# Kernel tuning notes

Hardware: AMD Instinct MI355X
Metric: run time of the kernel (lower is better)

## Reference

```python
import jax, jax.numpy as jnp
import numpy as np

B, T, D, H, L, W = 32, 512, 256, 8, 2, 10
NQ = 10000
HD = D // H


def setup_inputs():
    key = jax.random.key(0)
    ks = jax.random.split(key, 16)
    def n(k, shape, s=0.02):
        return jax.random.normal(k, shape, jnp.float32) * s
    return {
        "q": jax.random.randint(ks[0], (B, T), 0, NQ),
        "s": jax.random.randint(ks[1], (B, T), 0, 2),
        "q_embed": n(ks[2], (NQ + 1, D)),
        "s_embed": n(ks[3], (2, D)),
        "pos_embed": n(ks[4], (512, D)),
        "fusion_w": n(ks[5], (2 * D, D)),
        "fusion_b": jnp.zeros((D,), jnp.float32),
        "in_proj_w": n(ks[6], (L, D, 3 * D)),
        "in_proj_b": jnp.zeros((L, 3 * D), jnp.float32),
        "out_proj_w": n(ks[7], (L, D, D)),
        "out_proj_b": jnp.zeros((L, D), jnp.float32),
        "ln1_g": jnp.ones((L, D), jnp.float32),
        "ln1_b": jnp.zeros((L, D), jnp.float32),
        "ln2_g": jnp.ones((L, D), jnp.float32),
        "ln2_b": jnp.zeros((L, D), jnp.float32),
        "ff1_w": n(ks[8], (L, D, 4 * D)),
        "ff1_b": jnp.zeros((L, 4 * D), jnp.float32),
        "ff2_w": n(ks[9], (L, 4 * D, D)),
        "ff2_b": jnp.zeros((L, D), jnp.float32),
        "sw1": n(ks[10], (6, 32), 0.1),
        "sb1": jnp.zeros((32,), jnp.float32),
        "sw2": n(ks[11], (32, D // 4), 0.1),
        "sb2": jnp.zeros((D // 4,), jnp.float32),
        "cw1": n(ks[12], (D + D // 4, D)),
        "cb1": jnp.zeros((D,), jnp.float32),
        "cw2": n(ks[13], (D, 1)),
        "cb2": jnp.zeros((1,), jnp.float32),
    }


def _ln(x, g, b):
    mu = jnp.mean(x, -1, keepdims=True)
    var = jnp.mean(jnp.square(x - mu), -1, keepdims=True)
    return (x - mu) * jax.lax.rsqrt(var + 1e-5) * g + b


def _sliding_sum(x, w):
    # sum over trailing window of size w ending at each t, via prefix sums
    c = jnp.concatenate([jnp.zeros((x.shape[0], 1), x.dtype), jnp.cumsum(x, axis=1)], axis=1)
    t = jnp.arange(x.shape[1])
    return c[:, t + 1] - c[:, jnp.maximum(t + 1 - w, 0)]


def _stats(s, mask):
    # vectorized version of _extract_statistics (prefix-sum sliding windows)
    mf = mask.astype(jnp.float32)
    sf = s.astype(jnp.float32) * mf
    valid = _sliding_sum(mf, W)
    correct_rate = _sliding_sum(sf, W) / (valid + 1e-6)
    rc = _sliding_sum(mf, 5)
    recent_correct = _sliding_sum(sf, 5) / (rc + 1e-6)
    trans = ((s[:, 1:] != s[:, :-1]) & mask[:, 1:] & mask[:, :-1]).astype(jnp.float32)
    diff = jnp.concatenate([jnp.zeros((s.shape[0], 1), jnp.float32), trans], axis=1)
    change_rate = _sliding_sum(diff, W - 1) / (valid + 1e-6)
    # max consecutive equal run within each trailing window of size W
    sp = jnp.pad(s, ((0, 0), (W - 1, 0)))
    mp = jnp.pad(mask, ((0, 0), (W - 1, 0)))
    win_s = [sp[:, j:j + T] for j in range(W)]
    win_m = [mp[:, j:j + T] for j in range(W)]
    run = win_m[0].astype(jnp.float32)
    mx = run
    for j in range(1, W):  # fixed small window, not a data-dim loop
        eq = (win_s[j] == win_s[j - 1]) & win_m[j - 1]
        run = win_m[j].astype(jnp.float32) * (jnp.where(eq, run, 0.0) + 1.0)
        mx = jnp.maximum(mx, run)
    rel = jnp.broadcast_to(jnp.arange(T, dtype=jnp.float32) / max(T, 100), s.shape)
    cov = valid / W
    return jnp.stack([correct_rate, recent_correct, change_rate, mx / W, rel, cov], axis=-1)


def reference(q, s, q_embed, s_embed, pos_embed, fusion_w, fusion_b, in_proj_w, in_proj_b,
              out_proj_w, out_proj_b, ln1_g, ln1_b, ln2_g, ln2_b, ff1_w, ff1_b, ff2_w, ff2_b,
              sw1, sb1, sw2, sb2, cw1, cb1, cw2, cb2):
    mask = s >= 0
    qm = jnp.where(mask, q, 0)
    sm = jnp.where(mask, s, 0)
    h = jnp.concatenate([q_embed[qm], s_embed[sm]], axis=-1)  # [B,T,2D]
    h = jax.nn.relu(h @ fusion_w + fusion_b) + pos_embed[:T][None]
    causal = jnp.tril(jnp.ones((T, T), bool))
    allowed = causal[None, None] & mask[:, None, None, :]
    scale = 1.0 / (HD ** 0.5)
    for l in range(L):
        qkv = h @ in_proj_w[l] + in_proj_b[l]
        qh, kh, vh = jnp.split(qkv, 3, axis=-1)
        qh = qh.reshape(B, T, H, HD).transpose(0, 2, 1, 3)
        kh = kh.reshape(B, T, H, HD).transpose(0, 2, 1, 3)
        vh = vh.reshape(B, T, H, HD).transpose(0, 2, 1, 3)
        scores = jnp.einsum('bhqd,bhkd->bhqk', qh, kh) * scale
        scores = jnp.where(allowed, scores, -1e9)
        attn = jax.nn.softmax(scores, axis=-1)
        o = jnp.einsum('bhqk,bhkd->bhqd', attn, vh).transpose(0, 2, 1, 3).reshape(B, T, D)
        h = _ln(h + (o @ out_proj_w[l] + out_proj_b[l]), ln1_g[l], ln1_b[l])
        ff = jax.nn.gelu(h @ ff1_w[l] + ff1_b[l], approximate=False) @ ff2_w[l] + ff2_b[l]
        h = _ln(h + ff, ln2_g[l], ln2_b[l])
    sfeat = _stats(sm, mask)  # [B,T,6]
    semb = jax.nn.relu(sfeat @ sw1 + sb1) @ sw2 + sb2  # [B,T,D//4]
    comb = jnp.concatenate([h, semb], axis=-1)
    logits = (jax.nn.relu(comb @ cw1 + cb1) @ cw2 + cb2)[..., 0]
    return jnp.where(mask, logits, -1e9)
```

## Files before the change

### kernel.cpp

```cpp
#include <hip/hip_runtime.h>
#include <hip/hip_bf16.h>
#include <cmath>


using short8 = __attribute__((ext_vector_type(8))) short;
using short4v = __attribute__((ext_vector_type(4))) short;
using f32x4  = __attribute__((ext_vector_type(4))) float;

__device__ inline float gelu_f(float x) {
    return 0.5f * x * (1.0f + erff(x * 0.70710678118654752f));
}

__device__ inline short f2bf(float x) {
    union { float f; unsigned u; } v; v.f = x;
    return (short)((v.u + 0x7fffu + ((v.u >> 16) & 1u)) >> 16);
}

__device__ inline unsigned packbf(float lo, float hi) {
    union { float f; unsigned u; } a, b; a.f = lo; b.f = hi;
    unsigned ra = (a.u + 0x7fffu + ((a.u >> 16) & 1u)) >> 16;
    unsigned rb = (b.u + 0x7fffu + ((b.u >> 16) & 1u)) >> 16;
    return (rb << 16) | (ra & 0xffffu);
}

__device__ inline float wave_reduce_sum(float v) {
#pragma unroll
    for (int off = 32; off > 0; off >>= 1) v += __shfl_xor(v, off);
    return v;
}

#define GLOAD16(gp, lp) __builtin_amdgcn_global_load_lds( \
    (const __attribute__((address_space(1))) void*)(gp), \
    (__attribute__((address_space(3))) void*)(lp), 16, 0, 0)

__global__ __launch_bounds__(256) void transpose_all(
    const float* __restrict__ fusion_w, const float* __restrict__ in_proj_w,
    const float* __restrict__ out_proj_w, const float* __restrict__ ff1_w,
    const float* __restrict__ ff2_w, const float* __restrict__ cw1,
    short* __restrict__ wts)
{
    const int b0[10]      = {0,128,320,512,576,640,896,1152,1408,1664};
    const int Ks[10]      = {512,256,256,256,256,256,256,1024,1024,320};
    const int Ns[10]      = {256,768,768,256,256,1024,1024,256,256,256};
    const int sidx[10]    = {0,1,1,2,2,3,3,4,4,5};
    const size_t soff[10] = {0,0,196608,0,65536,0,262144,0,262144,0};
    const size_t doff[10] = {0,131072,327680,524288,589824,655360,917504,1179648,1441792,1703936};
    const float* srcs[6] = {fusion_w, in_proj_w, out_proj_w, ff1_w, ff2_w, cw1};

    int bid = blockIdx.x;
    int mi = 0;
    while (mi < 9 && bid >= b0[mi + 1]) ++mi;
    int bl = bid - b0[mi];
    int K = Ks[mi], N = Ns[mi];
    int tx = bl % (N >> 5), ty = bl / (N >> 5);
    const float* src = srcs[sidx[mi]] + soff[mi];
    short* dst = wts + doff[mi];

    __shared__ float tile[32][33];
    int c = threadIdx.x & 31, r = threadIdx.x >> 5;
#pragma unroll
    for (int i = 0; i < 4; ++i)
        tile[r + i * 8][c] = src[(size_t)(ty * 32 + r + i * 8) * N + tx * 32 + c];
    __syncthreads();
#pragma unroll
    for (int i = 0; i < 4; ++i)
        dst[(size_t)(tx * 32 + r + i * 8) * K + ty * 32 + c] = f2bf(tile[c][r + i * 8]);
}

__global__ __launch_bounds__(256) void embed_gather_bf16(
    const int* __restrict__ q, const int* __restrict__ s,
    const float* __restrict__ qe, const float* __restrict__ se,
    short* __restrict__ A)
{
    int e8 = blockIdx.x * 256 + threadIdx.x;
    int row = e8 >> 6;
    int k8 = (e8 & 63) << 3;
    int sv = s[row];
    bool mk = sv >= 0;
    const float* src = (k8 < 256) ? qe + (size_t)(mk ? q[row] : 0) * 256 + k8
                                  : se + (size_t)(mk ? sv : 0) * 256 + (k8 - 256);
    float4 v0 = *(const float4*)src;
    float4 v1 = *(const float4*)(src + 4);
    short8 o;
    o[0] = f2bf(v0.x); o[1] = f2bf(v0.y); o[2] = f2bf(v0.z); o[3] = f2bf(v0.w);
    o[4] = f2bf(v1.x); o[5] = f2bf(v1.y); o[6] = f2bf(v1.z); o[7] = f2bf(v1.w);
    *(short8*)(A + (size_t)row * 512 + k8) = o;
}

template<int EPI>
__global__ __launch_bounds__(512) void gemm512(
    const short* __restrict__ A, const short* __restrict__ A2,
    const short* __restrict__ Wt, const float* __restrict__ bias,
    float* __restrict__ hf, short* __restrict__ hb,
    short* __restrict__ oq, short* __restrict__ ok, short* __restrict__ ov,
    const float* __restrict__ gamma, const float* __restrict__ beta,
    const float* __restrict__ pos,
    const float* __restrict__ cw2, const float* __restrict__ cb2,
    const int* __restrict__ smask, float* __restrict__ outlog,
    int N, int K)
{
    const int tid = threadIdx.x, lane = tid & 63, wv = tid >> 6;
    const int lg = lane >> 4, lr = lane & 15;
    const int wr = wv >> 2, wc = wv & 3;
    const int m0 = blockIdx.y * 64, n0 = blockIdx.x * 256;

    __shared__ short As[2][2048];
    __shared__ short Bs[2][8192];
    __shared__ float redS[64][4];
    __shared__ float redQ[64][4];

    f32x4 acc[2][4] = {};
    const int nsteps = K >> 5;

    auto stage = [&](int buf, int step) {
        int k0 = step << 5;
        if (tid < 256) {
            int k = k0 + wv * 8;
            const short* srcA;
            if (EPI == 4) srcA = (k < 256) ? A  + (size_t)(m0 + lane) * 256 + k
                                           : A2 + (size_t)(m0 + lane) * 64 + (k - 256);
            else          srcA = A + (size_t)(m0 + lane) * K + k;
            GLOAD16(srcA, &As[buf][(wv * 64) * 8]);
        }
        {
            int g = tid >> 8, n = tid & 255;
            GLOAD16(Wt + (size_t)(n0 + n) * K + k0 + g * 8, &Bs[buf][(wv * 64) * 8]);
        }
        {
            int slot = tid + 512;
            int g = slot >> 8, n = slot & 255;
            GLOAD16(Wt + (size_t)(n0 + n) * K + k0 + g * 8, &Bs[buf][((wv + 8) * 64) * 8]);
        }
    };

    stage(0, 0);
    __syncthreads();
    for (int step = 0; step < nsteps; ++step) {
        int cur = step & 1;
        if (step + 1 < nsteps) stage(cur ^ 1, step + 1);
        short8 a[2], b[4];
#pragma unroll
        for (int i = 0; i < 2; ++i)
            a[i] = *(const short8*)&As[cur][(lg * 64 + wr * 32 + i * 16 + lr) * 8];
#pragma unroll
        for (int j = 0; j < 4; ++j)
            b[j] = *(const short8*)&Bs[cur][(lg * 256 + wc * 64 + j * 16 + lr) * 8];
#pragma unroll
        for (int i = 0; i < 2; ++i)
#pragma unroll
            for (int j = 0; j < 4; ++j)
                acc[i][j] = __builtin_amdgcn_mfma_f32_16x16x32_bf16(a[i], b[j], acc[i][j], 0, 0, 0);
        __syncthreads();
    }

    if (EPI == 0) {
#pragma unroll
        for (int i = 0; i < 2; ++i)
#pragma unroll
        for (int j = 0; j < 4; ++j)
#pragma unroll
        for (int r = 0; r < 4; ++r) {
            int row = m0 + wr * 32 + i * 16 + lg * 4 + r;
            int col = wc * 64 + j * 16 + lr;
            float x = acc[i][j][r] + bias[col];
            x = fmaxf(x, 0.f) + pos[(size_t)(row & 511) * 256 + col];
            hf[(size_t)row * 256 + col] = x;
            hb[(size_t)row * 256 + col] = f2bf(x);
        }
    } else if (EPI == 1) {
        const int sec = blockIdx.x;
#pragma unroll
        for (int i = 0; i < 2; ++i)
#pragma unroll
        for (int j = 0; j < 4; ++j)
#pragma unroll
        for (int r = 0; r < 4; ++r) {
            int row = m0 + wr * 32 + i * 16 + lg * 4 + r;
            int col = wc * 64 + j * 16 + lr;
            int t = row & 511, bg = row >> 9;
            int h = col >> 5, d = col & 31, bh = bg * 8 + h;
            short v = f2bf(acc[i][j][r] + bias[n0 + col]);
            if (sec == 0)      oq[((size_t)bh * 512 + t) * 32 + d] = v;
            else if (sec == 1) ok[((size_t)bh * 512 + t) * 32 + d] = v;
            else {
                int kl = t & 31;
                ov[(size_t)bh * 16384 + (size_t)(t >> 5) * 1024 +
                   (size_t)((kl >> 2) & 3) * 256 + d * 8 + (((kl & 3) << 1) | ((kl >> 4) & 1))] = v;
            }
        }
    } else if (EPI == 2) {
#pragma unroll
        for (int i = 0; i < 2; ++i)
#pragma unroll
        for (int j = 0; j < 4; ++j)
#pragma unroll
        for (int r = 0; r < 4; ++r) {
            int row = m0 + wr * 32 + i * 16 + lg * 4 + r;
            int col = n0 + wc * 64 + j * 16 + lr;
            float x = acc[i][j][r] + bias[col];
            oq[(size_t)row * N + col] = f2bf(gelu_f(x));
        }
    } else if (EPI == 3) {
        float ps[2][4], pq[2][4];
#pragma unroll
        for (int i = 0; i < 2; ++i)
#pragma unroll
        for (int r = 0; r < 4; ++r) { ps[i][r] = 0.f; pq[i][r] = 0.f; }
#pragma unroll
        for (int i = 0; i < 2; ++i)
#pragma unroll
        for (int j = 0; j < 4; ++j)
#pragma unroll
        for (int r = 0; r < 4; ++r) {
            int row = m0 + wr * 32 + i * 16 + lg * 4 + r;
            int col = wc * 64 + j * 16 + lr;
            float x = acc[i][j][r] + bias[col] + hf[(size_t)row * 256 + col];
            acc[i][j][r] = x;
            ps[i][r] += x; pq[i][r] += x * x;
        }
#pragma unroll
        for (int off = 1; off < 16; off <<= 1)
#pragma unroll
            for (int i = 0; i < 2; ++i)
#pragma unroll
            for (int r = 0; r < 4; ++r) {
                ps[i][r] += __shfl_xor(ps[i][r], off);
                pq[i][r] += __shfl_xor(pq[i][r], off);
            }
        if (lr == 0) {
#pragma unroll
            for (int i = 0; i < 2; ++i)
#pragma unroll
            for (int r = 0; r < 4; ++r) {
                int rl = wr * 32 + i * 16 + lg * 4 + r;
                redS[rl][wc] = ps[i][r]; redQ[rl][wc] = pq[i][r];
            }
        }
        __syncthreads();
#pragma unroll
        for (int i = 0; i < 2; ++i)
#pragma unroll
        for (int r = 0; r < 4; ++r) {
            int rl = wr * 32 + i * 16 + lg * 4 + r;
            int row = m0 + rl;
            float sm = redS[rl][0] + redS[rl][1] + redS[rl][2] + redS[rl][3];
            float sq = redQ[rl][0] + redQ[rl][1] + redQ[rl][2] + redQ[rl][3];
            float mu = sm * (1.f / 256.f);
            float var = sq * (1.f / 256.f) - mu * mu;
            float rstd = rsqrtf(var + 1e-5f);
#pragma unroll
            for (int j = 0; j < 4; ++j) {
                int col = wc * 64 + j * 16 + lr;
                float y = (acc[i][j][r] - mu) * rstd * gamma[col] + beta[col];
                hf[(size_t)row * 256 + col] = y;
                hb[(size_t)row * 256 + col] = f2bf(y);
            }
        }
    } else {
        float p[2][4];
#pragma unroll
        for (int i = 0; i < 2; ++i)
#pragma unroll
        for (int r = 0; r < 4; ++r) p[i][r] = 0.f;
#pragma unroll
        for (int i = 0; i < 2; ++i)
#pragma unroll
        for (int j = 0; j < 4; ++j)
#pragma unroll
        for (int r = 0; r < 4; ++r) {
            int col = wc * 64 + j * 16 + lr;
            float x = fmaxf(acc[i][j][r] + bias[col], 0.f);
            p[i][r] += x * cw2[col];
        }
#pragma unroll
        for (int off = 1; off < 16; off <<= 1)
#pragma unroll
            for (int i = 0; i < 2; ++i)
#pragma unroll
            for (int r = 0; r < 4; ++r) p[i][r] += __shfl_xor(p[i][r], off);
        if (lr == 0) {
#pragma unroll
            for (int i = 0; i < 2; ++i)
#pragma unroll
            for (int r = 0; r < 4; ++r)
                redS[wr * 32 + i * 16 + lg * 4 + r][wc] = p[i][r];
        }
        __syncthreads();
        if (tid < 64) {
            int row = m0 + tid;
            float v = redS[tid][0] + redS[tid][1] + redS[tid][2] + redS[tid][3] + cb2[0];
            outlog[row] = (smask[row] >= 0) ? v : -1e9f;
        }
    }
}

__global__ __launch_bounds__(256) void attn_mfma(
    const short* __restrict__ Qg, const short* __restrict__ Kg,
    const short* __restrict__ VTg, short* __restrict__ O)
{
    __shared__ unsigned Wp[4][16][20];
    const int bh = blockIdx.x >> 2, part = blockIdx.x & 3;
    const int b = bh >> 3, h = bh & 7;
    const int wv = threadIdx.x >> 6, lane = threadIdx.x & 63;
    const int lg = lane >> 4, lr = lane & 15;
    const int slot = part * 4 + wv;
    const short* Qbh = Qg + (size_t)bh * 16384;
    const short* Kbh = Kg + (size_t)bh * 16384;
    const short* Vbh = VTg + (size_t)bh * 16384;
    const float scale = 0.17677669529663687f;

    for (int half = 0; half < 2; ++half) {
        const int tile = half ? (31 - slot) : slot;
        const int q0 = tile << 4;
        short8 qa = *(const short8*)(Qbh + (size_t)(q0 + lr) * 32 + lg * 8);
        f32x4 o0 = {}, o1 = {};
        float l_[4] = {0.f, 0.f, 0.f, 0.f};
        const int nfull = q0 >> 5;

        for (int c = 0; c <= nfull; ++c) {
            int kc = c << 5;
            short8 kf0 = *(const short8*)(Kbh + (size_t)(kc + lr) * 32 + lg * 8);
            short8 kf1 = *(const short8*)(Kbh + (size_t)(kc + 16 + lr) * 32 + lg * 8);
            f32x4 s0 = {}, s1 = {};
            s0 = __builtin_amdgcn_mfma_f32_16x16x32_bf16(qa, kf0, s0, 0, 0, 0);
            s1 = __builtin_amdgcn_mfma_f32_16x16x32_bf16(qa, kf1, s1, 0, 0, 0);
            float p0[4], p1[4];
            if (c < nfull) {
#pragma unroll
                for (int r = 0; r < 4; ++r) {
                    p0[r] = __expf(s0[r] * scale);
                    p1[r] = __expf(s1[r] * scale);
                }
            } else {
#pragma unroll
                for (int r = 0; r < 4; ++r) {
                    int qq = q0 + lg * 4 + r;
                    p0[r] = (kc + lr)      > qq ? 0.f : __expf(s0[r] * scale);
                    p1[r] = (kc + 16 + lr) > qq ? 0.f : __expf(s1[r] * scale);
                }
            }
#pragma unroll
            for (int r = 0; r < 4; ++r) {
                l_[r] += p0[r] + p1[r];
                Wp[wv][lg * 4 + r][lr] = packbf(p0[r], p1[r]);
            }
            short8 pa = *(const short8*)&Wp[wv][lr][lg * 4];
            short8 vf0 = *(const short8*)(Vbh + (size_t)c * 1024 + lg * 256 + lr * 8);
            short8 vf1 = *(const short8*)(Vbh + (size_t)c * 1024 + lg * 256 + (lr + 16) * 8);
            o0 = __builtin_amdgcn_mfma_f32_16x16x32_bf16(pa, vf0, o0, 0, 0, 0);
            o1 = __builtin_amdgcn_mfma_f32_16x16x32_bf16(pa, vf1, o1, 0, 0, 0);
        }
#pragma unroll
        for (int off = 1; off < 16; off <<= 1)
#pragma unroll
            for (int r = 0; r < 4; ++r) l_[r] += __shfl_xor(l_[r], off);
#pragma unroll
        for (int r = 0; r < 4; ++r) {
            float inv = 1.f / l_[r];
            size_t ro = ((size_t)b * 512 + q0 + lg * 4 + r) * 256 + h * 32;
            O[ro + lr] = f2bf(o0[r] * inv);
            O[ro + 16 + lr] = f2bf(o1[r] * inv);
        }
    }
}

__global__ __launch_bounds__(512) void stats_kernel(
    const int* __restrict__ s, short* __restrict__ semb,
    const float* __restrict__ sw1, const float* __restrict__ sb1,
    const float* __restrict__ sw2, const float* __restrict__ sb2)
{
    __shared__ float sv_sh[512];
    __shared__ float m_sh[512];
    __shared__ float sw2_sh[2048];
    const int b = blockIdx.x;
    const int t = threadIdx.x;
    {
        int sval = s[b * 512 + t];
        bool mk = sval >= 0;
        sv_sh[t] = mk ? (float)sval : 0.f;
        m_sh[t] = mk ? 1.f : 0.f;
    }
    for (int i = t; i < 2048; i += 512) sw2_sh[i] = sw2[i];
    __syncthreads();

    float mf10 = 0, sf10 = 0, mf5 = 0, sf5 = 0, d9 = 0;
#pragma unroll
    for (int k = 0; k < 10; ++k) {
        int idx = t - k;
        if (idx >= 0) {
            float mv = m_sh[idx], sv = sv_sh[idx];
            mf10 += mv; sf10 += sv;
            if (k < 5) { mf5 += mv; sf5 += sv; }
            if (k < 9 && idx >= 1) {
                if (sv != sv_sh[idx - 1] && mv > 0.5f && m_sh[idx - 1] > 0.5f) d9 += 1.f;
            }
        }
    }
    float run, mx;
    {
        int x0 = t - 9;
        run = (x0 >= 0) ? m_sh[x0] : 0.f;
        mx = run;
#pragma unroll
        for (int j = 1; j < 10; ++j) {
            int xc = t + j - 9, xp = xc - 1;
            float sc = (xc >= 0) ? sv_sh[xc] : 0.f;
            float sp = (xp >= 0) ? sv_sh[xp] : 0.f;
            float mc = (xc >= 0) ? m_sh[xc] : 0.f;
            float mp = (xp >= 0) ? m_sh[xp] : 0.f;
            bool eq = (sc == sp) && (mp > 0.5f);
            run = (mc > 0.5f) ? ((eq ? run : 0.f) + 1.f) : 0.f;
            mx = fmaxf(mx, run);
        }
    }
    float f[6];
    f[0] = sf10 / (mf10 + 1e-6f);
    f[1] = sf5 / (mf5 + 1e-6f);
    f[2] = d9 / (mf10 + 1e-6f);
    f[3] = mx * 0.1f;
    f[4] = (float)t * (1.f / 512.f);
    f[5] = mf10 * 0.1f;

    float hid[32];
#pragma unroll
    for (int j2 = 0; j2 < 32; ++j2) {
        float a = sb1[j2];
#pragma unroll
        for (int i = 0; i < 6; ++i) a = fmaf(f[i], sw1[i * 32 + j2], a);
        hid[j2] = fmaxf(a, 0.f);
    }
    short* orow = semb + ((size_t)b * 512 + t) * 64;
    for (int c = 0; c < 64; c += 4) {
        float v0 = sb2[c], v1 = sb2[c + 1], v2 = sb2[c + 2], v3 = sb2[c + 3];
#pragma unroll
        for (int j2 = 0; j2 < 32; ++j2) {
            float hh = hid[j2];
            v0 = fmaf(hh, sw2_sh[j2 * 64 + c], v0);
            v1 = fmaf(hh, sw2_sh[j2 * 64 + c + 1], v1);
            v2 = fmaf(hh, sw2_sh[j2 * 64 + c + 2], v2);
            v3 = fmaf(hh, sw2_sh[j2 * 64 + c + 3], v3);
        }
        short4v o; o[0] = f2bf(v0); o[1] = f2bf(v1); o[2] = f2bf(v2); o[3] = f2bf(v3);
        *(short4v*)(orow + c) = o;
    }
}

extern "C" void kernel_launch(void* const* d_in, const int* in_sizes, int n_in,
                              void* d_out, int out_size, void* d_ws, size_t ws_size,
                              hipStream_t stream) {
    const int*   q         = (const int*)d_in[0];
    const int*   s         = (const int*)d_in[1];
    const float* q_embed   = (const float*)d_in[2];
    const float* s_embed   = (const float*)d_in[3];
    const float* pos_embed = (const float*)d_in[4];
    const float* fusion_w  = (const float*)d_in[5];
    const float* fusion_b  = (const float*)d_in[6];
    const float* in_proj_w = (const float*)d_in[7];
    const float* in_proj_b = (const float*)d_in[8];
    const float* out_proj_w= (const float*)d_in[9];
    const float* out_proj_b= (const float*)d_in[10];
    const float* ln1_g     = (const float*)d_in[11];
    const float* ln1_b     = (const float*)d_in[12];
    const float* ln2_g     = (const float*)d_in[13];
    const float* ln2_b     = (const float*)d_in[14];
    const float* ff1_w     = (const float*)d_in[15];
    const float* ff1_b     = (const float*)d_in[16];
    const float* ff2_w     = (const float*)d_in[17];
    const float* ff2_b     = (const float*)d_in[18];
    const float* sw1       = (const float*)d_in[19];
    const float* sb1       = (const float*)d_in[20];
    const float* sw2       = (const float*)d_in[21];
    const float* sb2       = (const float*)d_in[22];
    const float* cw1       = (const float*)d_in[23];
    const float* cb1       = (const float*)d_in[24];
    const float* cw2       = (const float*)d_in[25];
    const float* cb2       = (const float*)d_in[26];
    float* out = (float*)d_out;

    char* base = (char*)d_ws;
    float* hf   = (float*)(base);
    short* hb   = (short*)(base + 16777216);
    short* bufA = (short*)(base + 25165824);
    short* att  = (short*)(base + 58720256);
    short* Qg   = (short*)(base + 67108864);
    short* Kg   = (short*)(base + 75497472);
    short* VTg  = (short*)(base + 83886080);
    short* semb = (short*)(base + 92274688);
    short* wts  = (short*)(base + 94371840);

    const size_t W_FUSION = 0, W_INPROJ0 = 131072, W_INPROJ1 = 327680;
    const size_t W_OUTPROJ0 = 524288, W_OUTPROJ1 = 589824;
    const size_t W_FF1_0 = 655360, W_FF1_1 = 917504;
    const size_t W_FF2_0 = 1179648, W_FF2_1 = 1441792;
    const size_t W_CW1 = 1703936;

    transpose_all<<<1744, 256, 0, stream>>>(fusion_w, in_proj_w, out_proj_w,
                                            ff1_w, ff2_w, cw1, wts);
    embed_gather_bf16<<<4096, 256, 0, stream>>>(q, s, q_embed, s_embed, bufA);
    gemm512<0><<<dim3(1, 256), 512, 0, stream>>>(bufA, nullptr, wts + W_FUSION, fusion_b,
        hf, hb, nullptr, nullptr, nullptr, nullptr, nullptr, pos_embed,
        nullptr, nullptr, nullptr, nullptr, 256, 512);
    for (int l = 0; l < 2; ++l) {
        gemm512<1><<<dim3(3, 256), 512, 0, stream>>>(hb, nullptr,
            wts + (l ? W_INPROJ1 : W_INPROJ0), in_proj_b + l * 768,
            nullptr, nullptr, Qg, Kg, VTg, nullptr, nullptr, nullptr,
            nullptr, nullptr, nullptr, nullptr, 768, 256);
        attn_mfma<<<1024, 256, 0, stream>>>(Qg, Kg, VTg, att);
        gemm512<3><<<dim3(1, 256), 512, 0, stream>>>(att, nullptr,
            wts + (l ? W_OUTPROJ1 : W_OUTPROJ0), out_proj_b + l * 256,
            hf, hb, nullptr, nullptr, nullptr, ln1_g + l * 256, ln1_b + l * 256,
            nullptr, nullptr, nullptr, nullptr, nullptr, 256, 256);
        gemm512<2><<<dim3(4, 256), 512, 0, stream>>>(hb, nullptr,
            wts + (l ? W_FF1_1 : W_FF1_0), ff1_b + l * 1024,
            nullptr, nullptr, bufA, nullptr, nullptr, nullptr, nullptr, nullptr,
            nullptr, nullptr, nullptr, nullptr, 1024, 256);
        gemm512<3><<<dim3(1, 256), 512, 0, stream>>>(bufA, nullptr,
            wts + (l ? W_FF2_1 : W_FF2_0), ff2_b + l * 256,
            hf, hb, nullptr, nullptr, nullptr, ln2_g + l * 256, ln2_b + l * 256,
            nullptr, nullptr, nullptr, nullptr, nullptr, 256, 1024);
    }
    stats_kernel<<<32, 512, 0, stream>>>(s, semb, sw1, sb1, sw2, sb2);
    gemm512<4><<<dim3(1, 256), 512, 0, stream>>>(hb, semb, wts + W_CW1, cb1,
        nullptr, nullptr, nullptr, nullptr, nullptr, nullptr, nullptr, nullptr,
        cw2, cb2, s, out, 256, 320);
}
```

Measured before the change: 339.7 us.

## Rewrite GEMMs with triple-buffered pipeline, new tiles, and drop fp32 residual

Replaces the 512-thread double-buffered GEMM with a templated 256-thread kernel. It uses three LDS stages with explicit vmcnt waits and raw barriers, 128x128 or 64x256 tiles, and grouped block swizzling for L2 reuse. It also fuses the weight transpose and embedding gather into one prep launch. The fp32 residual copy of hidden state is removed, so residuals are now read back from the bf16 buffer. This cuts memory traffic at the cost of some residual precision, and the hand-written waitcnt values are brittle.

```diff
diff --git a/kernel.cpp b/kernel.cpp
--- a/kernel.cpp
+++ b/kernel.cpp
@@ -14,6 +14,11 @@
 __device__ inline short f2bf(float x) {
     union { float f; unsigned u; } v; v.f = x;
     return (short)((v.u + 0x7fffu + ((v.u >> 16) & 1u)) >> 16);
+}
+
+__device__ inline float bf2f(short v) {
+    union { unsigned u; float f; } x; x.u = ((unsigned)(unsigned short)v) << 16;
+    return x.f;
 }
 
 __device__ inline unsigned packbf(float lo, float hi) {
@@ -23,163 +28,173 @@
     return (rb << 16) | (ra & 0xffffu);
 }
 
-__device__ inline float wave_reduce_sum(float v) {
-#pragma unroll
-    for (int off = 32; off > 0; off >>= 1) v += __shfl_xor(v, off);
-    return v;
-}
-
 #define GLOAD16(gp, lp) __builtin_amdgcn_global_load_lds( \
     (const __attribute__((address_space(1))) void*)(gp), \
     (__attribute__((address_space(3))) void*)(lp), 16, 0, 0)
 
-__global__ __launch_bounds__(256) void transpose_all(
+#define WAITVM(n) asm volatile("s_waitcnt vmcnt(" #n ")" ::: "memory")
+
+__global__ __launch_bounds__(256) void prep_kernel(
     const float* __restrict__ fusion_w, const float* __restrict__ in_proj_w,
     const float* __restrict__ out_proj_w, const float* __restrict__ ff1_w,
     const float* __restrict__ ff2_w, const float* __restrict__ cw1,
-    short* __restrict__ wts)
-{
-    const int b0[10]      = {0,128,320,512,576,640,896,1152,1408,1664};
-    const int Ks[10]      = {512,256,256,256,256,256,256,1024,1024,320};
-    const int Ns[10]      = {256,768,768,256,256,1024,1024,256,256,256};
-    const int sidx[10]    = {0,1,1,2,2,3,3,4,4,5};
-    const size_t soff[10] = {0,0,196608,0,65536,0,262144,0,262144,0};
-    const size_t doff[10] = {0,131072,327680,524288,589824,655360,917504,1179648,1441792,1703936};
-    const float* srcs[6] = {fusion_w, in_proj_w, out_proj_w, ff1_w, ff2_w, cw1};
-
-    int bid = blockIdx.x;
-    int mi = 0;
-    while (mi < 9 && bid >= b0[mi + 1]) ++mi;
-    int bl = bid - b0[mi];
-    int K = Ks[mi], N = Ns[mi];
-    int tx = bl % (N >> 5), ty = bl / (N >> 5);
-    const float* src = srcs[sidx[mi]] + soff[mi];
-    short* dst = wts + doff[mi];
-
-    __shared__ float tile[32][33];
-    int c = threadIdx.x & 31, r = threadIdx.x >> 5;
-#pragma unroll
-    for (int i = 0; i < 4; ++i)
-        tile[r + i * 8][c] = src[(size_t)(ty * 32 + r + i * 8) * N + tx * 32 + c];
-    __syncthreads();
-#pragma unroll
-    for (int i = 0; i < 4; ++i)
-        dst[(size_t)(tx * 32 + r + i * 8) * K + ty * 32 + c] = f2bf(tile[c][r + i * 8]);
-}
-
-__global__ __launch_bounds__(256) void embed_gather_bf16(
+    short* __restrict__ wts,
     const int* __restrict__ q, const int* __restrict__ s,
     const float* __restrict__ qe, const float* __restrict__ se,
     short* __restrict__ A)
 {
-    int e8 = blockIdx.x * 256 + threadIdx.x;
-    int row = e8 >> 6;
-    int k8 = (e8 & 63) << 3;
-    int sv = s[row];
-    bool mk = sv >= 0;
-    const float* src = (k8 < 256) ? qe + (size_t)(mk ? q[row] : 0) * 256 + k8
-                                  : se + (size_t)(mk ? sv : 0) * 256 + (k8 - 256);
-    float4 v0 = *(const float4*)src;
-    float4 v1 = *(const float4*)(src + 4);
-    short8 o;
-    o[0] = f2bf(v0.x); o[1] = f2bf(v0.y); o[2] = f2bf(v0.z); o[3] = f2bf(v0.w);
-    o[4] = f2bf(v1.x); o[5] = f2bf(v1.y); o[6] = f2bf(v1.z); o[7] = f2bf(v1.w);
-    *(short8*)(A + (size_t)row * 512 + k8) = o;
-}
-
-template<int EPI>
-__global__ __launch_bounds__(512) void gemm512(
+    __shared__ float tile[32][33];
+    if (blockIdx.x < 1744) {
+        const int b0[10]      = {0,128,320,512,576,640,896,1152,1408,1664};
+        const int Ks[10]      = {512,256,256,256,256,256,256,1024,1024,320};
+        const int Ns[10]      = {256,768,768,256,256,1024,1024,256,256,256};
+        const int sidx[10]    = {0,1,1,2,2,3,3,4,4,5};
+        const size_t soff[10] = {0,0,196608,0,65536,0,262144,0,262144,0};
+        const size_t doff[10] = {0,131072,327680,524288,589824,655360,917504,1179648,1441792,1703936};
+        const float* srcs[6] = {fusion_w, in_proj_w, out_proj_w, ff1_w, ff2_w, cw1};
+        int bid = blockIdx.x;
+        int mi = 0;
+        while (mi < 9 && bid >= b0[mi + 1]) ++mi;
+        int bl = bid - b0[mi];
+        int K = Ks[mi], N = Ns[mi];
+        int tx = bl % (N >> 5), ty = bl / (N >> 5);
+        const float* src = srcs[sidx[mi]] + soff[mi];
+        short* dst = wts + doff[mi];
+        int c = threadIdx.x & 31, r = threadIdx.x >> 5;
+#pragma unroll
+        for (int i = 0; i < 4; ++i)
+            tile[r + i * 8][c] = src[(size_t)(ty * 32 + r + i * 8) * N + tx * 32 + c];
+        __syncthreads();
+#pragma unroll
+        for (int i = 0; i < 4; ++i)
+            dst[(size_t)(tx * 32 + r + i * 8) * K + ty * 32 + c] = f2bf(tile[c][r + i * 8]);
+    } else {
+        int e8 = (blockIdx.x - 1744) * 256 + threadIdx.x;
+        int row = e8 >> 6;
+        int k8 = (e8 & 63) << 3;
+        int sv = s[row];
+        bool mk = sv >= 0;
+        const float* src = (k8 < 256) ? qe + (size_t)(mk ? q[row] : 0) * 256 + k8
+                                      : se + (size_t)(mk ? sv : 0) * 256 + (k8 - 256);
+        float4 v0 = *(const float4*)src;
+        float4 v1 = *(const float4*)(src + 4);
+        short8 o;
+        o[0] = f2bf(v0.x); o[1] = f2bf(v0.y); o[2] = f2bf(v0.z); o[3] = f2bf(v0.w);
+        o[4] = f2bf(v1.x); o[5] = f2bf(v1.y); o[6] = f2bf(v1.z); o[7] = f2bf(v1.w);
+        *(short8*)(A + (size_t)row * 512 + k8) = o;
+    }
+}
+
+template<int EPI, int BM, int BN, int PANELS>
+__global__ __launch_bounds__(256, (BM == 128) ? 3 : 2) void gemm_pipe(
     const short* __restrict__ A, const short* __restrict__ A2,
     const short* __restrict__ Wt, const float* __restrict__ bias,
-    float* __restrict__ hf, short* __restrict__ hb,
-    short* __restrict__ oq, short* __restrict__ ok, short* __restrict__ ov,
+    short* __restrict__ hb, short* __restrict__ oq, short* __restrict__ ok,
+    short* __restrict__ ov,
     const float* __restrict__ gamma, const float* __restrict__ beta,
-    const float* __restrict__ pos,
-    const float* __restrict__ cw2, const float* __restrict__ cb2,
-    const int* __restrict__ smask, float* __restrict__ outlog,
-    int N, int K)
+    const float* __restrict__ pos, const float* __restrict__ cw2,
+    const float* __restrict__ cb2, const int* __restrict__ smask,
+    float* __restrict__ outlog, int N, int K)
 {
+    constexpr int WC = BN / 64;
+    constexpr int L = BM / 64 + BN / 64;
     const int tid = threadIdx.x, lane = tid & 63, wv = tid >> 6;
     const int lg = lane >> 4, lr = lane & 15;
-    const int wr = wv >> 2, wc = wv & 3;
-    const int m0 = blockIdx.y * 64, n0 = blockIdx.x * 256;
-
-    __shared__ short As[2][2048];
-    __shared__ short Bs[2][8192];
+    const int wr = wv / WC, wc = wv % WC;
+    const int bid = blockIdx.x;
+    const int p = (bid >> 3) % PANELS;
+    const int y = ((bid >> 3) / PANELS) * 8 + (bid & 7);
+    const int m0 = y * BM, n0 = p * BN;
+
+    __shared__ short As[3][BM * 32];
+    __shared__ short Bs[3][BN * 32];
     __shared__ float redS[64][4];
     __shared__ float redQ[64][4];
 
-    f32x4 acc[2][4] = {};
+    f32x4 acc[4][4] = {};
     const int nsteps = K >> 5;
 
     auto stage = [&](int buf, int step) {
         int k0 = step << 5;
-        if (tid < 256) {
-            int k = k0 + wv * 8;
-            const short* srcA;
-            if (EPI == 4) srcA = (k < 256) ? A  + (size_t)(m0 + lane) * 256 + k
-                                           : A2 + (size_t)(m0 + lane) * 64 + (k - 256);
-            else          srcA = A + (size_t)(m0 + lane) * K + k;
-            GLOAD16(srcA, &As[buf][(wv * 64) * 8]);
-        }
-        {
-            int g = tid >> 8, n = tid & 255;
-            GLOAD16(Wt + (size_t)(n0 + n) * K + k0 + g * 8, &Bs[buf][(wv * 64) * 8]);
-        }
-        {
-            int slot = tid + 512;
-            int g = slot >> 8, n = slot & 255;
-            GLOAD16(Wt + (size_t)(n0 + n) * K + k0 + g * 8, &Bs[buf][((wv + 8) * 64) * 8]);
+#pragma unroll
+        for (int i = 0; i < BM / 64; ++i) {
+            int slot = i * 256 + tid;
+            int g = slot / BM, m = slot % BM;
+            int k = k0 + g * 8;
+            const short* src;
+            if constexpr (EPI == 4)
+                src = (k < 256) ? A + (size_t)(m0 + m) * 256 + k
+                                : A2 + (size_t)(m0 + m) * 64 + (k - 256);
+            else
+                src = A + (size_t)(m0 + m) * K + k;
+            GLOAD16(src, &As[buf][slot * 8]);
+        }
+#pragma unroll
+        for (int i = 0; i < BN / 64; ++i) {
+            int slot = i * 256 + tid;
+            int g = slot / BN, n = slot % BN;
+            GLOAD16(Wt + (size_t)(n0 + n) * K + k0 + g * 8, &Bs[buf][slot * 8]);
         }
     };
 
     stage(0, 0);
-    __syncthreads();
-    for (int step = 0; step < nsteps; ++step) {
-        int cur = step & 1;
-        if (step + 1 < nsteps) stage(cur ^ 1, step + 1);
-        short8 a[2], b[4];
-#pragma unroll
-        for (int i = 0; i < 2; ++i)
-            a[i] = *(const short8*)&As[cur][(lg * 64 + wr * 32 + i * 16 + lr) * 8];
+    stage(1, 1);
+    int cur = 0;
+    for (int t = 0; t < nsteps; ++t) {
+        if (t + 2 < nsteps) {
+            int c2 = cur + 2; if (c2 >= 3) c2 -= 3;
+            stage(c2, t + 2);
+            if constexpr (L == 4) WAITVM(8); else WAITVM(10);
+        } else if (t + 1 < nsteps) {
+            if constexpr (L == 4) WAITVM(4); else WAITVM(5);
+        } else {
+            WAITVM(0);
+        }
+        __builtin_amdgcn_s_barrier();
+        __builtin_amdgcn_sched_barrier(0);
+        short8 a[4], b[4];
+#pragma unroll
+        for (int i = 0; i < 4; ++i)
+            a[i] = *(const short8*)&As[cur][(lg * BM + wr * 64 + i * 16 + lr) * 8];
 #pragma unroll
         for (int j = 0; j < 4; ++j)
-            b[j] = *(const short8*)&Bs[cur][(lg * 256 + wc * 64 + j * 16 + lr) * 8];
-#pragma unroll
-        for (int i = 0; i < 2; ++i)
+            b[j] = *(const short8*)&Bs[cur][(lg * BN + wc * 64 + j * 16 + lr) * 8];
+#pragma unroll
+        for (int i = 0; i < 4; ++i)
 #pragma unroll
             for (int j = 0; j < 4; ++j)
                 acc[i][j] = __builtin_amdgcn_mfma_f32_16x16x32_bf16(a[i], b[j], acc[i][j], 0, 0, 0);
-        __syncthreads();
-    }
-
-    if (EPI == 0) {
-#pragma unroll
-        for (int i = 0; i < 2; ++i)
+        __builtin_amdgcn_sched_barrier(0);
+        __builtin_amdgcn_s_barrier();
+        cur = (cur == 2) ? 0 : cur + 1;
+    }
+
+    if constexpr (EPI == 0) {
+#pragma unroll
+        for (int i = 0; i < 4; ++i)
 #pragma unroll
         for (int j = 0; j < 4; ++j)
 #pragma unroll
         for (int r = 0; r < 4; ++r) {
-            int row = m0 + wr * 32 + i * 16 + lg * 4 + r;
-            int col = wc * 64 + j * 16 + lr;
+            int row = m0 + wr * 64 + i * 16 + lg * 4 + r;
+            int col = n0 + wc * 64 + j * 16 + lr;
             float x = acc[i][j][r] + bias[col];
             x = fmaxf(x, 0.f) + pos[(size_t)(row & 511) * 256 + col];
-            hf[(size_t)row * 256 + col] = x;
             hb[(size_t)row * 256 + col] = f2bf(x);
         }
-    } else if (EPI == 1) {
-        const int sec = blockIdx.x;
-#pragma unroll
-        for (int i = 0; i < 2; ++i)
+    } else if constexpr (EPI == 1) {
+#pragma unroll
+        for (int i = 0; i < 4; ++i)
 #pragma unroll
         for (int j = 0; j < 4; ++j)
 #pragma unroll
         for (int r = 0; r < 4; ++r) {
-            int row = m0 + wr * 32 + i * 16 + lg * 4 + r;
-            int col = wc * 64 + j * 16 + lr;
+            int row = m0 + wr * 64 + i * 16 + lg * 4 + r;
+            int gcol = n0 + wc * 64 + j * 16 + lr;
             int t = row & 511, bg = row >> 9;
-            int h = col >> 5, d = col & 31, bh = bg * 8 + h;
-            short v = f2bf(acc[i][j][r] + bias[n0 + col]);
+            int sec = gcol >> 8, cc = gcol & 255;
+            int h = cc >> 5, d = cc & 31, bh = bg * 8 + h;
+            short v = f2bf(acc[i][j][r] + bias[gcol]);
             if (sec == 0)      oq[((size_t)bh * 512 + t) * 32 + d] = v;
             else if (sec == 1) ok[((size_t)bh * 512 + t) * 32 + d] = v;
             else {
@@ -188,40 +203,40 @@
                    (size_t)((kl >> 2) & 3) * 256 + d * 8 + (((kl & 3) << 1) | ((kl >> 4) & 1))] = v;
             }
         }
-    } else if (EPI == 2) {
-#pragma unroll
-        for (int i = 0; i < 2; ++i)
+    } else if constexpr (EPI == 2) {
+#pragma unroll
+        for (int i = 0; i < 4; ++i)
 #pragma unroll
         for (int j = 0; j < 4; ++j)
 #pragma unroll
         for (int r = 0; r < 4; ++r) {
-            int row = m0 + wr * 32 + i * 16 + lg * 4 + r;
-            int col = n0 + wc * 64 + j * 16 + lr;
-            float x = acc[i][j][r] + bias[col];
-            oq[(size_t)row * N + col] = f2bf(gelu_f(x));
-        }
-    } else if (EPI == 3) {
-        float ps[2][4], pq[2][4];
-#pragma unroll
-        for (int i = 0; i < 2; ++i)
+            int row = m0 + wr * 64 + i * 16 + lg * 4 + r;
+            int gcol = n0 + wc * 64 + j * 16 + lr;
+            float x = acc[i][j][r] + bias[gcol];
+            oq[(size_t)row * N + gcol] = f2bf(gelu_f(x));
+        }
+    } else if constexpr (EPI == 3) {
+        float ps[4][4], pq[4][4];
+#pragma unroll
+        for (int i = 0; i < 4; ++i)
 #pragma unroll
         for (int r = 0; r < 4; ++r) { ps[i][r] = 0.f; pq[i][r] = 0.f; }
 #pragma unroll
-        for (int i = 0; i < 2; ++i)
+        for (int i = 0; i < 4; ++i)
 #pragma unroll
         for (int j = 0; j < 4; ++j)
 #pragma unroll
         for (int r = 0; r < 4; ++r) {
-            int row = m0 + wr * 32 + i * 16 + lg * 4 + r;
+            int row = m0 + i * 16 + lg * 4 + r;
             int col = wc * 64 + j * 16 + lr;
-            float x = acc[i][j][r] + bias[col] + hf[(size_t)row * 256 + col];
+            float x = acc[i][j][r] + bias[col] + bf2f(hb[(size_t)row * 256 + col]);
             acc[i][j][r] = x;
             ps[i][r] += x; pq[i][r] += x * x;
         }
 #pragma unroll
         for (int off = 1; off < 16; off <<= 1)
 #pragma unroll
-            for (int i = 0; i < 2; ++i)
+            for (int i = 0; i < 4; ++i)
 #pragma unroll
             for (int r = 0; r < 4; ++r) {
                 ps[i][r] += __shfl_xor(ps[i][r], off);
@@ -229,19 +244,19 @@
             }
         if (lr == 0) {
 #pragma unroll
-            for (int i = 0; i < 2; ++i)
+            for (int i = 0; i < 4; ++i)
 #pragma unroll
             for (int r = 0; r < 4; ++r) {
-                int rl = wr * 32 + i * 16 + lg * 4 + r;
+                int rl = i * 16 + lg * 4 + r;
                 redS[rl][wc] = ps[i][r]; redQ[rl][wc] = pq[i][r];
             }
         }
         __syncthreads();
 #pragma unroll
-        for (int i = 0; i < 2; ++i)
-#pragma unroll
-        for (int r = 0; r < 4; ++r) {
-            int rl = wr * 32 + i * 16 + lg * 4 + r;
+        for (int i = 0; i < 4; ++i)
+#pragma unroll
+        for (int r = 0; r < 4; ++r) {
+            int rl = i * 16 + lg * 4 + r;
             int row = m0 + rl;
             float sm = redS[rl][0] + redS[rl][1] + redS[rl][2] + redS[rl][3];
             float sq = redQ[rl][0] + redQ[rl][1] + redQ[rl][2] + redQ[rl][3];
@@ -251,39 +266,38 @@
 #pragma unroll
             for (int j = 0; j < 4; ++j) {
                 int col = wc * 64 + j * 16 + lr;
-                float y = (acc[i][j][r] - mu) * rstd * gamma[col] + beta[col];
-                hf[(size_t)row * 256 + col] = y;
-                hb[(size_t)row * 256 + col] = f2bf(y);
+                float yv = (acc[i][j][r] - mu) * rstd * gamma[col] + beta[col];
+                hb[(size_t)row * 256 + col] = f2bf(yv);
             }
         }
     } else {
-        float p[2][4];
-#pragma unroll
-        for (int i = 0; i < 2; ++i)
-#pragma unroll
-        for (int r = 0; r < 4; ++r) p[i][r] = 0.f;
-#pragma unroll
-        for (int i = 0; i < 2; ++i)
+        float pa[4][4];
+#pragma unroll
+        for (int i = 0; i < 4; ++i)
+#pragma unroll
+        for (int r = 0; r < 4; ++r) pa[i][r] = 0.f;
+#pragma unroll
+        for (int i = 0; i < 4; ++i)
 #pragma unroll
         for (int j = 0; j < 4; ++j)
 #pragma unroll
         for (int r = 0; r < 4; ++r) {
             int col = wc * 64 + j * 16 + lr;
             float x = fmaxf(acc[i][j][r] + bias[col], 0.f);
-            p[i][r] += x * cw2[col];
+            pa[i][r] += x * cw2[col];
         }
 #pragma unroll
         for (int off = 1; off < 16; off <<= 1)
 #pragma unroll
-            for (int i = 0; i < 2; ++i)
-#pragma unroll
-            for (int r = 0; r < 4; ++r) p[i][r] += __shfl_xor(p[i][r], off);
+            for (int i = 0; i < 4; ++i)
+#pragma unroll
+            for (int r = 0; r < 4; ++r) pa[i][r] += __shfl_xor(pa[i][r], off);
         if (lr == 0) {
 #pragma unroll
-            for (int i = 0; i < 2; ++i)
+            for (int i = 0; i < 4; ++i)
 #pragma unroll
             for (int r = 0; r < 4; ++r)
-                redS[wr * 32 + i * 16 + lg * 4 + r][wc] = p[i][r];
+                redS[i * 16 + lg * 4 + r][wc] = pa[i][r];
         }
         __syncthreads();
         if (tid < 64) {
@@ -478,15 +492,14 @@
     float* out = (float*)d_out;
 
     char* base = (char*)d_ws;
-    float* hf   = (float*)(base);
-    short* hb   = (short*)(base + 16777216);
-    short* bufA = (short*)(base + 25165824);
-    short* att  = (short*)(base + 58720256);
-    short* Qg   = (short*)(base + 67108864);
-    short* Kg   = (short*)(base + 75497472);
-    short* VTg  = (short*)(base + 83886080);
-    short* semb = (short*)(base + 92274688);
-    short* wts  = (short*)(base + 94371840);
+    short* hb   = (short*)(base);
+    short* bufA = (short*)(base + 8388608);
+    short* att  = (short*)(base + 41943040);
+    short* Qg   = (short*)(base + 50331648);
+    short* Kg   = (short*)(base + 58720256);
+    short* VTg  = (short*)(base + 67108864);
+    short* semb = (short*)(base + 75497472);
+    short* wts  = (short*)(base + 77594624);
 
     const size_t W_FUSION = 0, W_INPROJ0 = 131072, W_INPROJ1 = 327680;
     const size_t W_OUTPROJ0 = 524288, W_OUTPROJ1 = 589824;
@@ -494,33 +507,33 @@
     const size_t W_FF2_0 = 1179648, W_FF2_1 = 1441792;
     const size_t W_CW1 = 1703936;
 
-    transpose_all<<<1744, 256, 0, stream>>>(fusion_w, in_proj_w, out_proj_w,
-                                            ff1_w, ff2_w, cw1, wts);
-    embed_gather_bf16<<<4096, 256, 0, stream>>>(q, s, q_embed, s_embed, bufA);
-    gemm512<0><<<dim3(1, 256), 512, 0, stream>>>(bufA, nullptr, wts + W_FUSION, fusion_b,
-        hf, hb, nullptr, nullptr, nullptr, nullptr, nullptr, pos_embed,
-        nullptr, nullptr, nullptr, nullptr, 256, 512);
+    prep_kernel<<<5840, 256, 0, stream>>>(fusion_w, in_proj_w, out_proj_w,
+                                          ff1_w, ff2_w, cw1, wts,
+                                          q, s, q_embed, s_embed, bufA);
+    gemm_pipe<0, 128, 128, 2><<<256, 256, 0, stream>>>(bufA, nullptr,
+        wts + W_FUSION, fusion_b, hb, nullptr, nullptr, nullptr,
+        nullptr, nullptr, pos_embed, nullptr, nullptr, nullptr, nullptr, 256, 512);
     for (int l = 0; l < 2; ++l) {
-        gemm512<1><<<dim3(3, 256), 512, 0, stream>>>(hb, nullptr,
+        gemm_pipe<1, 128, 128, 6><<<768, 256, 0, stream>>>(hb, nullptr,
             wts + (l ? W_INPROJ1 : W_INPROJ0), in_proj_b + l * 768,
-            nullptr, nullptr, Qg, Kg, VTg, nullptr, nullptr, nullptr,
-            nullptr, nullptr, nullptr, nullptr, 768, 256);
+            nullptr, Qg, Kg, VTg, nullptr, nullptr, nullptr, nullptr, nullptr,
+            nullptr, nullptr, 768, 256);
         attn_mfma<<<1024, 256, 0, stream>>>(Qg, Kg, VTg, att);
-        gemm512<3><<<dim3(1, 256), 512, 0, stream>>>(att, nullptr,
+        gemm_pipe<3, 64, 256, 1><<<256, 256, 0, stream>>>(att, nullptr,
             wts + (l ? W_OUTPROJ1 : W_OUTPROJ0), out_proj_b + l * 256,
-            hf, hb, nullptr, nullptr, nullptr, ln1_g + l * 256, ln1_b + l * 256,
+            hb, nullptr, nullptr, nullptr, ln1_g + l * 256, ln1_b + l * 256,
             nullptr, nullptr, nullptr, nullptr, nullptr, 256, 256);
-        gemm512<2><<<dim3(4, 256), 512, 0, stream>>>(hb, nullptr,
+        gemm_pipe<2, 128, 128, 8><<<1024, 256, 0, stream>>>(hb, nullptr,
             wts + (l ? W_FF1_1 : W_FF1_0), ff1_b + l * 1024,
-            nullptr, nullptr, bufA, nullptr, nullptr, nullptr, nullptr, nullptr,
+            nullptr, bufA, nullptr, nullptr, nullptr, nullptr, nullptr,
             nullptr, nullptr, nullptr, nullptr, 1024, 256);
-        gemm512<3><<<dim3(1, 256), 512, 0, stream>>>(bufA, nullptr,
+        gemm_pipe<3, 64, 256, 1><<<256, 256, 0, stream>>>(bufA, nullptr,
             wts + (l ? W_FF2_1 : W_FF2_0), ff2_b + l * 256,
-            hf, hb, nullptr, nullptr, nullptr, ln2_g + l * 256, ln2_b + l * 256,
+            hb, nullptr, nullptr, nullptr, ln2_g + l * 256, ln2_b + l * 256,
             nullptr, nullptr, nullptr, nullptr, nullptr, 256, 1024);
     }
     stats_kernel<<<32, 512, 0, stream>>>(s, semb, sw1, sb1, sw2, sb2);
-    gemm512<4><<<dim3(1, 256), 512, 0, stream>>>(hb, semb, wts + W_CW1, cb1,
-        nullptr, nullptr, nullptr, nullptr, nullptr, nullptr, nullptr, nullptr,
-        cw2, cb2, s, out, 256, 320);
-}
+    gemm_pipe<4, 64, 256, 1><<<256, 256, 0, stream>>>(hb, semb,
+        wts + W_CW1, cb1, nullptr, nullptr, nullptr, nullptr, nullptr, nullptr,
+        nullptr, cw2, cb2, s, out, 256, 320);
+}
```

After: 335.4 us. About the same (-1.3%).
